# Performance work log

Measured on AMD Instinct MI355X. Metric: run time of the kernel, lower is better.

## Reference

```python
import jax, jax.numpy as jnp
import numpy as np

LN_EPS = 1e-5

def setup_inputs() -> dict:
    key = jax.random.key(0)
    ks = jax.random.split(key, 4)
    B, C, L, P = 16, 512, 8192, 128
    return {
        "x": jax.random.normal(ks[0], (B, C, L), dtype=jnp.float32),
        "conv_mask_w": jax.random.normal(ks[1], (C,), dtype=jnp.float32) * (1.0 / np.sqrt(C)),
        "conv_mask_b": jnp.zeros((1,), dtype=jnp.float32),
        "w1": jax.random.normal(ks[2], (P, C), dtype=jnp.float32) * (1.0 / np.sqrt(C)),
        "b1": jnp.zeros((P,), dtype=jnp.float32),
        "ln_w": jnp.ones((P,), dtype=jnp.float32),
        "ln_b": jnp.zeros((P,), dtype=jnp.float32),
        "w2": jax.random.normal(ks[3], (C, P), dtype=jnp.float32) * (1.0 / np.sqrt(P)),
        "b2": jnp.zeros((C,), dtype=jnp.float32),
    }

def reference(x, conv_mask_w, conv_mask_b, w1, b1, ln_w, ln_b, w2, b2):
    # x: [B, C, L]
    # --- spatial_pool (pooling_type='att') ---
    # conv_mask: 1x1 Conv1d C->1 => per-position score
    scores = jnp.einsum('bcl,c->bl', x, conv_mask_w) + conv_mask_b  # [B, L]
    attn = jax.nn.softmax(scores, axis=-1)                          # softmax over L
    context = jnp.einsum('bcl,bl->bc', x, attn)                     # [B, C]
    # --- channel_add_conv: 1x1 conv -> LayerNorm([P,1]) -> ReLU -> 1x1 conv ---
    t = jnp.einsum('pc,bc->bp', w1, context) + b1                   # [B, P]
    mu = jnp.mean(t, axis=-1, keepdims=True)
    var = jnp.mean(jnp.square(t - mu), axis=-1, keepdims=True)
    t = (t - mu) * jax.lax.rsqrt(var + LN_EPS) * ln_w + ln_b
    t = jax.nn.relu(t)
    add_term = jnp.einsum('cp,bp->bc', w2, t) + b2                  # [B, C]
    return x + add_term[:, :, None]
```

## Files before the change

### kernel.cpp

```cpp
#include <hip/hip_runtime.h>
#include <math.h>

#define B 16
#define C 512
#define L 8192
#define PP 128
#define TL 32
#define TPB 8
#define NB (L / (TL * TPB))
#define LN_EPS 1e-5f

typedef float fx4 __attribute__((ext_vector_type(4)));

__global__ __launch_bounds__(1024, 8) void k_fused(
    const float* __restrict__ x, const float* __restrict__ cw,
    float* __restrict__ part_pc, float* __restrict__ part_m, float* __restrict__ part_z) {
  const int b = blockIdx.y;
  const int blk = blockIdx.x;
  const int tid = threadIdx.x;
  const int q = tid & 7;
  const int r = tid >> 3;
  const int lane = tid & 63;
  const int w = tid >> 6;

  __shared__ float scw[C];
  __shared__ float sred[16][32];
  __shared__ float pw[TL];
  __shared__ float s_resc;
  __shared__ float s_m, s_z;

  for (int c = tid; c < C; c += 1024) scw[c] = cw[c];
  if (tid == 0) { s_m = -INFINITY; s_z = 0.f; }

  float pc_acc[4] = {0.f, 0.f, 0.f, 0.f};
  const size_t xbase = (size_t)b * C * L;

  for (int t = 0; t < TPB; ++t) {
    const int l0 = (blk * TPB + t) * TL;
    const float4* xb4 = (const float4*)(x + xbase + l0);

    __syncthreads();

    float4 xv[4];
    float sp[4] = {0.f, 0.f, 0.f, 0.f};
    #pragma unroll
    for (int i = 0; i < 4; ++i) {
      const int c = r + 128 * i;
      const float4 v = xb4[(size_t)c * (L / 4) + q];
      xv[i] = v;
      const float wc = scw[c];
      sp[0] += v.x * wc; sp[1] += v.y * wc; sp[2] += v.z * wc; sp[3] += v.w * wc;
    }
    #pragma unroll
    for (int m = 8; m <= 32; m <<= 1) {
      sp[0] += __shfl_xor(sp[0], m);
      sp[1] += __shfl_xor(sp[1], m);
      sp[2] += __shfl_xor(sp[2], m);
      sp[3] += __shfl_xor(sp[3], m);
    }
    if (lane < 8) {
      sred[w][4 * lane + 0] = sp[0];
      sred[w][4 * lane + 1] = sp[1];
      sred[w][4 * lane + 2] = sp[2];
      sred[w][4 * lane + 3] = sp[3];
    }
    __syncthreads();

    if (tid < 32) {
      float s = 0.f;
      #pragma unroll
      for (int ww = 0; ww < 16; ++ww) s += sred[ww][tid];
      float m = s;
      #pragma unroll
      for (int off = 16; off; off >>= 1) m = fmaxf(m, __shfl_xor(m, off, 32));
      const float mold = s_m;
      const float mnew = fmaxf(mold, m);
      const float p = __expf(s - mnew);
      float z = p;
      #pragma unroll
      for (int off = 16; off; off >>= 1) z += __shfl_xor(z, off, 32);
      pw[tid] = p;
      if (tid == 0) {
        const float resc = __expf(mold - mnew);
        s_resc = resc;
        s_z = s_z * resc + z;
        s_m = mnew;
      }
    }
    __syncthreads();

    const float resc = s_resc;
    const float w0 = pw[4 * q + 0], w1 = pw[4 * q + 1];
    const float w2 = pw[4 * q + 2], w3 = pw[4 * q + 3];
    #pragma unroll
    for (int i = 0; i < 4; ++i) {
      float pv = xv[i].x * w0 + xv[i].y * w1 + xv[i].z * w2 + xv[i].w * w3;
      #pragma unroll
      for (int m = 1; m <= 4; m <<= 1) pv += __shfl_xor(pv, m);
      pc_acc[i] = pc_acc[i] * resc + pv;
    }
  }

  if (q == 0) {
    float* dst = part_pc + ((size_t)(b * NB + blk)) * C;
    #pragma unroll
    for (int i = 0; i < 4; ++i) dst[r + 128 * i] = pc_acc[i];
  }
  if (tid == 0) {
    part_m[b * NB + blk] = s_m;
    part_z[b * NB + blk] = s_z;
  }
}

__global__ void k_tail(const float* __restrict__ part_pc, const float* __restrict__ part_m,
                       const float* __restrict__ part_z,
                       const float* __restrict__ w1, const float* __restrict__ b1,
                       const float* __restrict__ lnw, const float* __restrict__ lnb,
                       const float* __restrict__ w2, const float* __restrict__ b2,
                       float* __restrict__ add_term) {
  const int b = blockIdx.x;
  const int tid = threadIdx.x;
  __shared__ float se[NB];
  __shared__ float sctx[C];
  __shared__ float st[PP];

  if (tid < 64) {
    const float m = (tid < NB) ? part_m[b * NB + tid] : -INFINITY;
    float M = m;
    #pragma unroll
    for (int off = 16; off; off >>= 1) M = fmaxf(M, __shfl_xor(M, off, 32));
    const float e = (tid < NB) ? __expf(m - M) : 0.f;
    float Z = (tid < NB) ? part_z[b * NB + tid] * e : 0.f;
    #pragma unroll
    for (int off = 16; off; off >>= 1) Z += __shfl_xor(Z, off, 32);
    if (tid < NB) se[tid] = e / Z;
  }
  __syncthreads();

  float acc = 0.f;
  const float* pp = part_pc + (size_t)b * NB * C + tid;
  #pragma unroll
  for (int t = 0; t < NB; ++t) acc += pp[(size_t)t * C] * se[t];
  sctx[tid] = acc;
  __syncthreads();

  {
    const int p = tid >> 2;
    const int q = tid & 3;
    const float* w1r = w1 + (size_t)p * C + q * 128;
    const float* cx = &sctx[q * 128];
    float a = 0.f;
    #pragma unroll 8
    for (int cc = 0; cc < 128; ++cc) a += w1r[cc] * cx[cc];
    a += __shfl_xor(a, 1);
    a += __shfl_xor(a, 2);
    if (q == 0) st[p] = a + b1[p];
  }
  __syncthreads();

  float tv = 0.f;
  if (tid < PP) {
    float mu = 0.f;
    #pragma unroll 8
    for (int pi = 0; pi < PP; ++pi) mu += st[pi];
    mu *= (1.f / PP);
    float var = 0.f;
    #pragma unroll 8
    for (int pi = 0; pi < PP; ++pi) { const float d = st[pi] - mu; var += d * d; }
    var *= (1.f / PP);
    tv = (st[tid] - mu) * rsqrtf(var + LN_EPS) * lnw[tid] + lnb[tid];
    tv = fmaxf(tv, 0.f);
  }
  __syncthreads();
  if (tid < PP) st[tid] = tv;
  __syncthreads();

  float a2 = b2[tid];
  const float* w2r = w2 + (size_t)tid * PP;
  #pragma unroll 8
  for (int pi = 0; pi < PP; ++pi) a2 += w2r[pi] * st[pi];
  add_term[b * C + tid] = a2;
}

__global__ void k_add(const float* __restrict__ x, const float* __restrict__ at,
                      float* __restrict__ out) {
  const int bc = blockIdx.x;
  const float a = at[bc];
  const fx4* xr = (const fx4*)(x + (size_t)bc * L);
  fx4* orow = (fx4*)(out + (size_t)bc * L);
  #pragma unroll 4
  for (int i = threadIdx.x; i < L / 4; i += 256) {
    fx4 v = xr[i];
    v = v + a;
    __builtin_nontemporal_store(v, &orow[i]);
  }
}

extern "C" void kernel_launch(void* const* d_in, const int* in_sizes, int n_in,
                              void* d_out, int out_size, void* d_ws, size_t ws_size,
                              hipStream_t stream) {
  const float* x   = (const float*)d_in[0];
  const float* cw  = (const float*)d_in[1];
  const float* w1  = (const float*)d_in[3];
  const float* b1  = (const float*)d_in[4];
  const float* lnw = (const float*)d_in[5];
  const float* lnb = (const float*)d_in[6];
  const float* w2  = (const float*)d_in[7];
  const float* b2  = (const float*)d_in[8];
  float* out = (float*)d_out;

  char* ws = (char*)d_ws;
  float* part_pc  = (float*)ws;
  float* part_m   = (float*)(ws + (size_t)B * NB * C * 4);
  float* part_z   = part_m + B * NB;
  float* add_term = part_z + B * NB;

  k_fused<<<dim3(NB, B), 1024, 0, stream>>>(x, cw, part_pc, part_m, part_z);
  k_tail<<<dim3(B), C, 0, stream>>>(part_pc, part_m, part_z,
                                    w1, b1, lnw, lnb, w2, b2, add_term);
  k_add<<<dim3(B * C), 256, 0, stream>>>(x, add_term, out);
}
```

Measured before the change: 153.2 us.

## Restructure fused pooling kernel to 512 threads with per-channel context pass

Rewrites the fused score/context kernel to use 512 threads. Scores are computed with scalar strided loads over 32 channels per thread group, and each thread then computes one channel's context by re-reading its 32-element row with vector loads. This removes the shuffle reductions and the four-way register tiling. In exchange, x is read twice per tile (relying on cache) and the second pass uses per-row accesses that are less coalesced.

```diff
diff --git a/kernel.cpp b/kernel.cpp
--- a/kernel.cpp
+++ b/kernel.cpp
@@ -5,71 +5,51 @@
 #define C 512
 #define L 8192
 #define PP 128
-#define TL 32
+#define TILE_L 32
 #define TPB 8
-#define NB (L / (TL * TPB))
+#define NB (L / (TILE_L * TPB))
 #define LN_EPS 1e-5f
 
 typedef float fx4 __attribute__((ext_vector_type(4)));
 
-__global__ __launch_bounds__(1024, 8) void k_fused(
+__global__ __launch_bounds__(512) void k_fused(
     const float* __restrict__ x, const float* __restrict__ cw,
     float* __restrict__ part_pc, float* __restrict__ part_m, float* __restrict__ part_z) {
   const int b = blockIdx.y;
   const int blk = blockIdx.x;
   const int tid = threadIdx.x;
-  const int q = tid & 7;
-  const int r = tid >> 3;
-  const int lane = tid & 63;
-  const int w = tid >> 6;
+  const int l_ofs = tid & 31;
+  const int rg = tid >> 5;
 
   __shared__ float scw[C];
   __shared__ float sred[16][32];
-  __shared__ float pw[TL];
-  __shared__ float s_resc;
-  __shared__ float s_m, s_z;
+  __shared__ float pw[TILE_L];
+  __shared__ float s_m, s_z, s_resc;
 
-  for (int c = tid; c < C; c += 1024) scw[c] = cw[c];
+  scw[tid] = cw[tid];
   if (tid == 0) { s_m = -INFINITY; s_z = 0.f; }
 
-  float pc_acc[4] = {0.f, 0.f, 0.f, 0.f};
+  float pc_acc = 0.f;
   const size_t xbase = (size_t)b * C * L;
 
   for (int t = 0; t < TPB; ++t) {
-    const int l0 = (blk * TPB + t) * TL;
-    const float4* xb4 = (const float4*)(x + xbase + l0);
-
+    const int l0 = (blk * TPB + t) * TILE_L;
     __syncthreads();
 
-    float4 xv[4];
-    float sp[4] = {0.f, 0.f, 0.f, 0.f};
+    float ps = 0.f;
+    const float* xp = x + xbase + l0 + l_ofs;
     #pragma unroll
-    for (int i = 0; i < 4; ++i) {
-      const int c = r + 128 * i;
-      const float4 v = xb4[(size_t)c * (L / 4) + q];
-      xv[i] = v;
-      const float wc = scw[c];
-      sp[0] += v.x * wc; sp[1] += v.y * wc; sp[2] += v.z * wc; sp[3] += v.w * wc;
+    for (int i = 0; i < 32; ++i) {
+      const int c = (rg << 5) + i;
+      ps += xp[(size_t)c * L] * scw[c];
     }
-    #pragma unroll
-    for (int m = 8; m <= 32; m <<= 1) {
-      sp[0] += __shfl_xor(sp[0], m);
-      sp[1] += __shfl_xor(sp[1], m);
-      sp[2] += __shfl_xor(sp[2], m);
-      sp[3] += __shfl_xor(sp[3], m);
-    }
-    if (lane < 8) {
-      sred[w][4 * lane + 0] = sp[0];
-      sred[w][4 * lane + 1] = sp[1];
-      sred[w][4 * lane + 2] = sp[2];
-      sred[w][4 * lane + 3] = sp[3];
-    }
+    sred[rg][l_ofs] = ps;
     __syncthreads();
 
     if (tid < 32) {
       float s = 0.f;
       #pragma unroll
-      for (int ww = 0; ww < 16; ++ww) s += sred[ww][tid];
+      for (int g = 0; g < 16; ++g) s += sred[g][tid];
       float m = s;
       #pragma unroll
       for (int off = 16; off; off >>= 1) m = fmaxf(m, __shfl_xor(m, off, 32));
@@ -89,23 +69,17 @@
     }
     __syncthreads();
 
-    const float resc = s_resc;
-    const float w0 = pw[4 * q + 0], w1 = pw[4 * q + 1];
-    const float w2 = pw[4 * q + 2], w3 = pw[4 * q + 3];
+    const fx4* xr4 = (const fx4*)(x + xbase + (size_t)tid * L + l0);
+    float pv = 0.f;
     #pragma unroll
-    for (int i = 0; i < 4; ++i) {
-      float pv = xv[i].x * w0 + xv[i].y * w1 + xv[i].z * w2 + xv[i].w * w3;
-      #pragma unroll
-      for (int m = 1; m <= 4; m <<= 1) pv += __shfl_xor(pv, m);
-      pc_acc[i] = pc_acc[i] * resc + pv;
+    for (int j = 0; j < 8; ++j) {
+      const fx4 v = xr4[j];
+      pv += v.x * pw[4 * j] + v.y * pw[4 * j + 1] + v.z * pw[4 * j + 2] + v.w * pw[4 * j + 3];
     }
+    pc_acc = pc_acc * s_resc + pv;
   }
 
-  if (q == 0) {
-    float* dst = part_pc + ((size_t)(b * NB + blk)) * C;
-    #pragma unroll
-    for (int i = 0; i < 4; ++i) dst[r + 128 * i] = pc_acc[i];
-  }
+  part_pc[(size_t)(b * NB + blk) * C + tid] = pc_acc;
   if (tid == 0) {
     part_m[b * NB + blk] = s_m;
     part_z[b * NB + blk] = s_z;
@@ -215,7 +189,7 @@
   float* part_z   = part_m + B * NB;
   float* add_term = part_z + B * NB;
 
-  k_fused<<<dim3(NB, B), 1024, 0, stream>>>(x, cw, part_pc, part_m, part_z);
+  k_fused<<<dim3(NB, B), 512, 0, stream>>>(x, cw, part_pc, part_m, part_z);
   k_tail<<<dim3(B), C, 0, stream>>>(part_pc, part_m, part_z,
                                     w1, b1, lnw, lnb, w2, b2, add_term);
   k_add<<<dim3(B * C), 256, 0, stream>>>(x, add_term, out);
```

Result: slower. 180.2 us (+17.6%).
